# Optimization experiments

Hardware: AMD Instinct MI355X
Metric: run time of the kernel (lower is better)

Reference implementation:

```python
import jax, jax.numpy as jnp
import numpy as np

N, E = 50000, 1600000
IN, HID, HEADS, OUT = 128, 32, 4, 32
NEG_SLOPE = 0.2  # PyG GATConv default leaky_relu slope


def _glorot(k, shape):
    fan = shape[0] + shape[-1]
    return jax.random.normal(k, shape, dtype=jnp.float32) * np.sqrt(2.0 / fan).astype(np.float32)


def setup_inputs() -> dict:
    key = jax.random.key(0)
    ks = jax.random.split(key, 16)
    x = jax.random.normal(ks[0], (N, IN), dtype=jnp.float32)
    edge_index = jax.random.randint(ks[1], (2, E), 0, N, dtype=jnp.int32)
    # layer 0: in -> heads*hid, concat
    W0 = _glorot(ks[2], (IN, HEADS * HID))
    as0 = _glorot(ks[3], (HEADS, HID)); ad0 = _glorot(ks[4], (HEADS, HID))
    b0 = jnp.zeros((HEADS * HID,), jnp.float32)
    # layer 1: heads*hid -> heads*hid, concat
    W1 = _glorot(ks[5], (HEADS * HID, HEADS * HID))
    as1 = _glorot(ks[6], (HEADS, HID)); ad1 = _glorot(ks[7], (HEADS, HID))
    b1 = jnp.zeros((HEADS * HID,), jnp.float32)
    # layer 2: heads*hid -> out, heads=1, concat=False
    W2 = _glorot(ks[8], (HEADS * HID, OUT))
    as2 = _glorot(ks[9], (1, OUT)); ad2 = _glorot(ks[10], (1, OUT))
    b2 = jnp.zeros((OUT,), jnp.float32)
    return dict(x=x, edge_index=edge_index, W0=W0, as0=as0, ad0=ad0, b0=b0,
                W1=W1, as1=as1, ad1=ad1, b1=b1, W2=W2, as2=as2, ad2=ad2, b2=b2)


def gat_layer(x, src, dst, W, a_src, a_dst, b, heads, out_ch, concat):
    # linear transform per head: [N, heads, out_ch]
    h = (x @ W).reshape(N, heads, out_ch)
    # per-node attention half-logits: [N, heads]
    alpha_src = jnp.einsum('nhc,hc->nh', h, a_src)
    alpha_dst = jnp.einsum('nhc,hc->nh', h, a_dst)
    # per-edge logits (edge j -> i): [E', heads]
    logits = jax.nn.leaky_relu(alpha_src[src] + alpha_dst[dst], NEG_SLOPE)
    # segment softmax over incoming edges of each destination node
    m = jax.ops.segment_max(logits, dst, num_segments=N)
    e = jnp.exp(logits - m[dst])
    denom = jax.ops.segment_sum(e, dst, num_segments=N)
    alpha = e / denom[dst]
    # weighted message scatter-add: [N, heads, out_ch]
    out = jax.ops.segment_sum(h[src] * alpha[:, :, None], dst, num_segments=N)
    out = out.reshape(N, heads * out_ch) if concat else out.mean(axis=1)
    return out + b, alpha


def reference(x, edge_index, W0, as0, ad0, b0, W1, as1, ad1, b1, W2, as2, ad2, b2):
    # add self loops (PyG add_self_loops=True)
    loops = jnp.arange(N, dtype=edge_index.dtype)
    src = jnp.concatenate([edge_index[0], loops])
    dst = jnp.concatenate([edge_index[1], loops])

    h, alpha0 = gat_layer(x, src, dst, W0, as0, ad0, b0, HEADS, HID, True)
    h = jax.nn.elu(h)  # dropout inactive in eval mode
    h, _ = gat_layer(h, src, dst, W1, as1, ad1, b1, HEADS, HID, True)
    h = jax.nn.elu(h)
    out, _ = gat_layer(h, src, dst, W2, as2, ad2, b2, 1, OUT, False)
    return alpha0, out
```

## Files before the change

### kernel.cpp

```cpp
#include <hip/hip_runtime.h>
#include <math.h>

#define NN 50000
#define NEG 0.2f
#define TILE 4096

typedef __attribute__((ext_vector_type(8))) short short8;
typedef __attribute__((ext_vector_type(4))) float f32x4;

__device__ __forceinline__ unsigned short f2bf(float f){
    unsigned u = __float_as_uint(f);
    u += 0x7fffu + ((u >> 16) & 1u);
    return (unsigned short)(u >> 16);
}
__device__ __forceinline__ float bf2f(unsigned short v){
    return __uint_as_float(((unsigned)v) << 16);
}

__device__ __forceinline__ int excl_scan_256(int v, int* buf, int tid){
    buf[tid] = v;
    __syncthreads();
#pragma unroll
    for (int off = 1; off < 256; off <<= 1){
        int t = (tid >= off) ? buf[tid - off] : 0;
        __syncthreads();
        buf[tid] += t;
        __syncthreads();
    }
    return buf[tid] - v;
}

__global__ __launch_bounds__(256) void k_binning(const int* __restrict__ ei, int E,
        int* __restrict__ bucketCount, unsigned* __restrict__ tmp){
    __shared__ unsigned stage[TILE];
    __shared__ int hist[256], sbuf[256], exs[256], cur[256], gbase[256];
    int tid = threadIdx.x;
    int EP = E + NN;
    int tileBase = blockIdx.x * TILE;
    int cnt = min(TILE, EP - tileBase);

    hist[tid] = 0;
    __syncthreads();

    unsigned packed[16];
#pragma unroll
    for (int k = 0; k < 16; ++k){
        int e = tileBase + tid + (k << 8);
        unsigned p = 0xffffffffu;
        if (e < EP){
            int s, d;
            if (e < E){ s = ei[e]; d = ei[E + e]; } else { s = e - E; d = s; }
            p = ((unsigned)d << 16) | (unsigned)s;
            atomicAdd(&hist[d >> 8], 1);
        }
        packed[k] = p;
    }
    __syncthreads();
    int h = hist[tid];
    int ex = excl_scan_256(h, sbuf, tid);
    exs[tid] = ex;
    cur[tid] = ex;
    __syncthreads();
#pragma unroll
    for (int k = 0; k < 16; ++k){
        unsigned p = packed[k];
        if (p != 0xffffffffu){
            int b = p >> 24;
            int pos = atomicAdd(&cur[b], 1);
            stage[pos] = p;
        }
    }
    gbase[tid] = atomicAdd(&bucketCount[tid], h);
    __syncthreads();
    for (int i = tid; i < cnt; i += 256){
        unsigned p = stage[i];
        int b = p >> 24;
        tmp[(b << 14) + gbase[b] + (i - exs[b])] = p;
    }
}

__global__ __launch_bounds__(256) void k_bucket_csr(int EP,
        const int* __restrict__ bucketCount, const unsigned* __restrict__ tmp,
        int* __restrict__ row_ptr, unsigned short* __restrict__ ssrc){
    __shared__ int sbuf[256], deg[256], cur[256];
    __shared__ int baseSh, nSh;
    int b = blockIdx.x;
    int tid = threadIdx.x;
    int c = bucketCount[tid];
    int exb = excl_scan_256(c, sbuf, tid);
    if (tid == b){ baseSh = exb; nSh = c; }
    deg[tid] = 0;
    __syncthreads();
    int base = baseSh, n = nSh;
    const unsigned* tb = tmp + ((size_t)b << 14);
    for (int i = tid; i < n; i += 256)
        atomicAdd(&deg[(tb[i] >> 16) & 255], 1);
    __syncthreads();
    int d = deg[tid];
    int dx = excl_scan_256(d, sbuf, tid);
    cur[tid] = dx;
    int dst = (b << 8) + tid;
    if (dst < NN) row_ptr[dst] = base + dx;
    if (b == 0 && tid == 0) row_ptr[NN] = EP;
    __syncthreads();
    for (int i = tid; i < n; i += 256){
        unsigned p = tb[i];
        int pos = atomicAdd(&cur[(p >> 16) & 255], 1);
        ssrc[base + pos] = (unsigned short)(p & 0xffffu);
    }
}

__global__ void k_packW(const float* __restrict__ W0, const float* __restrict__ W1,
                        const float* __restrict__ W2,
                        unsigned short* __restrict__ h0, unsigned short* __restrict__ l0,
                        unsigned short* __restrict__ h1, unsigned short* __restrict__ l1,
                        unsigned short* __restrict__ h2, unsigned short* __restrict__ l2){
    int t = blockIdx.x * 256 + threadIdx.x;
    const float* W; unsigned short *ph, *pl; int Ncol; int u;
    if (t < 16384){ W = W0; ph = h0; pl = l0; Ncol = 128; u = t; }
    else if (t < 32768){ W = W1; ph = h1; pl = l1; Ncol = 128; u = t - 16384; }
    else if (t < 36864){ W = W2; ph = h2; pl = l2; Ncol = 32;  u = t - 32768; }
    else return;
    int n = u >> 7, k = u & 127;
    float f = W[k * Ncol + n];
    unsigned short hi = f2bf(f);
    unsigned short lo = f2bf(f - bf2f(hi));
    ph[n * 128 + k] = hi;
    pl[n * 128 + k] = lo;
}

template<int NT, int HH>
__global__ __launch_bounds__(256) void k_gemm_mfma(
        const float* __restrict__ A,
        const unsigned short* __restrict__ Bhi,
        const unsigned short* __restrict__ Blo,
        float* __restrict__ C, unsigned short* __restrict__ Cbf,
        const float* __restrict__ a_s,
        const float* __restrict__ a_d,
        float* __restrict__ asrc, float* __restrict__ adst,
        float* __restrict__ asrc_i, float* __restrict__ adst_i, int M){
    const int Ncol = NT * 16;
    int wave = threadIdx.x >> 6;
    int lane = threadIdx.x & 63;
    int r    = lane & 15;
    int oct  = lane >> 4;
    int rowBase = blockIdx.x * 64 + wave * 16;

    f32x4 acc[NT];
#pragma unroll
    for (int c = 0; c < NT; ++c) acc[c] = (f32x4){0.f, 0.f, 0.f, 0.f};

    int lrow = rowBase + r; if (lrow > M - 1) lrow = M - 1;
    const float* arow = A + (size_t)lrow * 128;

    for (int t = 0; t < 4; ++t){
        int k0 = t * 32 + oct * 8;
        float4 a0 = *(const float4*)&arow[k0];
        float4 a1 = *(const float4*)&arow[k0 + 4];
        float av[8] = {a0.x, a0.y, a0.z, a0.w, a1.x, a1.y, a1.z, a1.w};
        short8 ahi, alo;
#pragma unroll
        for (int j = 0; j < 8; ++j){
            unsigned short h = f2bf(av[j]);
            unsigned short l = f2bf(av[j] - bf2f(h));
            ahi[j] = (short)h; alo[j] = (short)l;
        }
#pragma unroll
        for (int c = 0; c < NT; ++c){
            short8 bhi = *(const short8*)&Bhi[(c * 16 + r) * 128 + k0];
            short8 blo = *(const short8*)&Blo[(c * 16 + r) * 128 + k0];
            acc[c] = __builtin_amdgcn_mfma_f32_16x16x32_bf16(ahi, bhi, acc[c], 0, 0, 0);
            acc[c] = __builtin_amdgcn_mfma_f32_16x16x32_bf16(alo, bhi, acc[c], 0, 0, 0);
            acc[c] = __builtin_amdgcn_mfma_f32_16x16x32_bf16(ahi, blo, acc[c], 0, 0, 0);
        }
    }
#pragma unroll
    for (int c = 0; c < NT; ++c){
#pragma unroll
        for (int reg = 0; reg < 4; ++reg){
            int row = rowBase + oct * 4 + reg;
            if (row < M){
                int colg = c * 16 + r;
                float v = acc[c][reg];
                if (C)   C[(size_t)row * Ncol + colg] = v;
                if (Cbf) Cbf[(size_t)(colg >> 5) * ((size_t)M * 32)
                             + (size_t)row * 32 + (colg & 31)] = f2bf(v);
            }
        }
    }

    float as_v[NT], ad_v[NT];
#pragma unroll
    for (int c = 0; c < NT; ++c){
        as_v[c] = a_s[c * 16 + r];
        ad_v[c] = a_d[c * 16 + r];
    }
    float vs[HH * 4], vd[HH * 4];
#pragma unroll
    for (int h = 0; h < HH; ++h)
#pragma unroll
        for (int reg = 0; reg < 4; ++reg){
            vs[h * 4 + reg] = acc[2 * h][reg] * as_v[2 * h]
                            + acc[2 * h + 1][reg] * as_v[2 * h + 1];
            vd[h * 4 + reg] = acc[2 * h][reg] * ad_v[2 * h]
                            + acc[2 * h + 1][reg] * ad_v[2 * h + 1];
        }
#pragma unroll
    for (int off = 1; off < 16; off <<= 1){
#pragma unroll
        for (int k = 0; k < HH * 4; ++k){
            vs[k] += __shfl_xor(vs[k], off);
            vd[k] += __shfl_xor(vd[k], off);
        }
    }
    if (HH == 4){
        int reg = r & 3, hd = r >> 2;
        int row = rowBase + oct * 4 + reg;
        if (row < M){
            asrc[hd * M + row] = vs[hd * 4 + reg];
            adst[hd * M + row] = vd[hd * 4 + reg];
            if (asrc_i){
                asrc_i[row * 4 + hd] = vs[hd * 4 + reg];
                adst_i[row * 4 + hd] = vd[hd * 4 + reg];
            }
        }
    } else {
        int reg = r & 3;
        int row = rowBase + oct * 4 + reg;
        if (row < M){
            if (r < 4)       asrc[row] = vs[reg];
            else if (r < 8)  adst[row] = vd[reg];
        }
    }
}

__global__ __launch_bounds__(256) void k_aggh4(
        const uint4* __restrict__ hb4,
        const float* __restrict__ asrc,
        const float* __restrict__ adst,
        const int* __restrict__ row_ptr, const unsigned short* __restrict__ ssrc,
        const float* __restrict__ bias, float* __restrict__ outp,
        float* __restrict__ gdenom, int writeStats){
    int b  = blockIdx.x;
    int h  = (b >> 1) & 3;
    int kh = (b >> 3) * 2 + (b & 1);
    int wave = threadIdx.x >> 6;
    int lane = threadIdx.x & 63;
    int ns = lane >> 4;
    int g  = (lane >> 2) & 3;
    int q  = lane & 3;
    int i  = kh * 16 + wave * 4 + ns;
    bool valid = (i < NN);
    int iv = valid ? i : NN - 1;
    int lo = row_ptr[iv], hi = row_ptr[iv + 1];
    float adv = adst[h * NN + iv];
    const uint4* hp = hb4 + (size_t)h * ((size_t)NN * 4);
    const float* ap = asrc + h * NN;

    float acc[8];
#pragma unroll
    for (int k = 0; k < 8; ++k) acc[k] = 0.f;
    float dsum = 0.f;

#define AGH_FMA(AA, GV) {                                                     \
        acc[0] += (AA) * __uint_as_float((GV).x << 16);                       \
        acc[1] += (AA) * __uint_as_float((GV).x & 0xffff0000u);               \
        acc[2] += (AA) * __uint_as_float((GV).y << 16);                       \
        acc[3] += (AA) * __uint_as_float((GV).y & 0xffff0000u);               \
        acc[4] += (AA) * __uint_as_float((GV).z << 16);                       \
        acc[5] += (AA) * __uint_as_float((GV).z & 0xffff0000u);               \
        acc[6] += (AA) * __uint_as_float((GV).w << 16);                       \
        acc[7] += (AA) * __uint_as_float((GV).w & 0xffff0000u); }
#define AGH_ONE(JJ) {                                                         \
        float lg_ = ap[(JJ)] + adv;                                           \
        lg_ = fmaxf(lg_, NEG * lg_);                                          \
        float a_ = __expf(lg_);                                               \
        dsum += a_;                                                           \
        uint4 gv_ = hp[(JJ) * 4u + (unsigned)q];                              \
        AGH_FMA(a_, gv_) }

    int idx = lo;
    if (lo & 1){
        if (g == 0){ unsigned j = ssrc[lo]; AGH_ONE(j) }
        idx = lo + 1;
    }
    for (; idx + 16 <= hi; idx += 16){
        unsigned pA = *(const unsigned*)&ssrc[idx + 2 * g];
        unsigned pB = *(const unsigned*)&ssrc[idx + 8 + 2 * g];
        unsigned j0 = pA & 0xffffu, j1 = pA >> 16;
        unsigned j2 = pB & 0xffffu, j3 = pB >> 16;
        float s0 = ap[j0], s1 = ap[j1], s2 = ap[j2], s3 = ap[j3];
        uint4 v0 = hp[j0 * 4u + (unsigned)q];
        uint4 v1 = hp[j1 * 4u + (unsigned)q];
        uint4 v2 = hp[j2 * 4u + (unsigned)q];
        uint4 v3 = hp[j3 * 4u + (unsigned)q];
        float lg0 = s0 + adv; lg0 = fmaxf(lg0, NEG * lg0);
        float lg1 = s1 + adv; lg1 = fmaxf(lg1, NEG * lg1);
        float lg2 = s2 + adv; lg2 = fmaxf(lg2, NEG * lg2);
        float lg3 = s3 + adv; lg3 = fmaxf(lg3, NEG * lg3);
        float a0 = __expf(lg0), a1 = __expf(lg1);
        float a2 = __expf(lg2), a3 = __expf(lg3);
        dsum += (a0 + a1) + (a2 + a3);
        AGH_FMA(a0, v0)
        AGH_FMA(a1, v1)
        AGH_FMA(a2, v2)
        AGH_FMA(a3, v3)
    }
    if (idx + 8 <= hi){
        unsigned pA = *(const unsigned*)&ssrc[idx + 2 * g];
        unsigned j0 = pA & 0xffffu, j1 = pA >> 16;
        float s0 = ap[j0], s1 = ap[j1];
        uint4 v0 = hp[j0 * 4u + (unsigned)q];
        uint4 v1 = hp[j1 * 4u + (unsigned)q];
        float lg0 = s0 + adv; lg0 = fmaxf(lg0, NEG * lg0);
        float lg1 = s1 + adv; lg1 = fmaxf(lg1, NEG * lg1);
        float a0 = __expf(lg0), a1 = __expf(lg1);
        dsum += a0 + a1;
        AGH_FMA(a0, v0)
        AGH_FMA(a1, v1)
        idx += 8;
    }
    {
        int k0 = idx + 2 * g, k1 = k0 + 1;
        if (k0 < hi){ unsigned j = ssrc[k0]; AGH_ONE(j) }
        if (k1 < hi){ unsigned j = ssrc[k1]; AGH_ONE(j) }
    }
#undef AGH_ONE
#undef AGH_FMA
#pragma unroll
    for (int k = 0; k < 8; ++k){
        acc[k] += __shfl_xor(acc[k], 4);
        acc[k] += __shfl_xor(acc[k], 8);
    }
    dsum += __shfl_xor(dsum, 4);
    dsum += __shfl_xor(dsum, 8);

    if (writeStats && g == 0 && q == 0 && valid)
        gdenom[i * 4 + h] = dsum;

    if (g == 0 && valid){
        float rs = 1.f / dsum;
        int c0 = h * 32 + q * 8;
        float4 bA = *(const float4*)&bias[c0];
        float4 bB = *(const float4*)&bias[c0 + 4];
        float o[8] = {acc[0] * rs + bA.x, acc[1] * rs + bA.y,
                      acc[2] * rs + bA.z, acc[3] * rs + bA.w,
                      acc[4] * rs + bB.x, acc[5] * rs + bB.y,
                      acc[6] * rs + bB.z, acc[7] * rs + bB.w};
#pragma unroll
        for (int k = 0; k < 8; ++k)
            o[k] = (o[k] > 0.f) ? o[k] : (__expf(o[k]) - 1.f);
        *(float4*)&outp[(size_t)i * 128 + c0]     = make_float4(o[0], o[1], o[2], o[3]);
        *(float4*)&outp[(size_t)i * 128 + c0 + 4] = make_float4(o[4], o[5], o[6], o[7]);
    }
}

__global__ void k_alpha0(const int* __restrict__ ei, int E,
                         const float4* __restrict__ asrc4, const float4* __restrict__ adst4,
                         const float4* __restrict__ gd4, float4* __restrict__ out){
    int e = blockIdx.x * 256 + threadIdx.x;
    int EP = E + NN;
    if (e >= EP) return;
    int s, d;
    if (e < E){ s = ei[e]; d = ei[E + e]; } else { s = e - E; d = s; }
    float4 as = asrc4[s], ad = adst4[d], dn = gd4[d];
    float4 r;
    float lg;
    lg = as.x + ad.x; lg = fmaxf(lg, NEG * lg); r.x = __expf(lg) / dn.x;
    lg = as.y + ad.y; lg = fmaxf(lg, NEG * lg); r.y = __expf(lg) / dn.y;
    lg = as.z + ad.z; lg = fmaxf(lg, NEG * lg); r.z = __expf(lg) / dn.z;
    lg = as.w + ad.w; lg = fmaxf(lg, NEG * lg); r.w = __expf(lg) / dn.w;
    out[e] = r;
}

__global__ __launch_bounds__(256) void k_agg1s(
        const float4* __restrict__ h24,
        const float* __restrict__ asrc, const float* __restrict__ adst,
        const int* __restrict__ row_ptr, const unsigned short* __restrict__ ssrc,
        const float* __restrict__ bias, float* __restrict__ outp){
    int wave = (blockIdx.x * 256 + threadIdx.x) >> 6;
    int lane = threadIdx.x & 63;
    if (wave >= NN) return;
    int i = wave;
    int lo = row_ptr[i], hi = row_ptr[i + 1];
    int g = lane >> 3;
    int q = lane & 7;
    float adv = adst[i];

    float acc[4] = {0.f, 0.f, 0.f, 0.f};
    float dsum = 0.f;

#define AGG1_ONE(JJ) {                                                        \
        float lg_ = asrc[(JJ)] + adv;                                         \
        lg_ = fmaxf(lg_, NEG * lg_);                                          \
        float a_ = __expf(lg_);                                               \
        dsum += a_;                                                           \
        float4 v_ = h24[(JJ) * 8u + (unsigned)q];                             \
        acc[0] += a_ * v_.x; acc[1] += a_ * v_.y;                             \
        acc[2] += a_ * v_.z; acc[3] += a_ * v_.w; }

    int idx = lo;
    if (lo & 1){
        if (g == 0){ unsigned j = ssrc[lo]; AGG1_ONE(j) }
        idx = lo + 1;
    }
    for (; idx + 16 <= hi; idx += 16){
        unsigned pair = *(const unsigned*)&ssrc[idx + 2 * g];
        unsigned j0 = pair & 0xffffu, j1 = pair >> 16;
        float s0 = asrc[j0];
        float s1 = asrc[j1];
        float4 v0 = h24[j0 * 8u + (unsigned)q];
        float4 v1 = h24[j1 * 8u + (unsigned)q];
        float lg0 = s0 + adv; lg0 = fmaxf(lg0, NEG * lg0);
        float lg1 = s1 + adv; lg1 = fmaxf(lg1, NEG * lg1);
        float a0 = __expf(lg0), a1 = __expf(lg1);
        dsum += a0 + a1;
        acc[0] += a0 * v0.x; acc[1] += a0 * v0.y;
        acc[2] += a0 * v0.z; acc[3] += a0 * v0.w;
        acc[0] += a1 * v1.x; acc[1] += a1 * v1.y;
        acc[2] += a1 * v1.z; acc[3] += a1 * v1.w;
    }
    {
        int k0 = idx + 2 * g, k1 = k0 + 1;
        if (k0 < hi){ unsigned j = ssrc[k0]; AGG1_ONE(j) }
        if (k1 < hi){ unsigned j = ssrc[k1]; AGG1_ONE(j) }
    }
#undef AGG1_ONE
#pragma unroll
    for (int k = 0; k < 4; ++k){
        acc[k] += __shfl_xor(acc[k], 8);
        acc[k] += __shfl_xor(acc[k], 16);
        acc[k] += __shfl_xor(acc[k], 32);
    }
    dsum += __shfl_xor(dsum, 8);
    dsum += __shfl_xor(dsum, 16);
    dsum += __shfl_xor(dsum, 32);
    if (g == 0){
        float rs = 1.f / dsum;
        float4 b = *(const float4*)&bias[q * 4];
        *(float4*)&outp[(size_t)i * 32 + q * 4] =
            make_float4(acc[0] * rs + b.x, acc[1] * rs + b.y,
                        acc[2] * rs + b.z, acc[3] * rs + b.w);
    }
}

extern "C" void kernel_launch(void* const* d_in, const int* in_sizes, int n_in,
                              void* d_out, int out_size, void* d_ws, size_t ws_size,
                              hipStream_t stream){
    const float* x   = (const float*)d_in[0];
    const int*   ei  = (const int*)  d_in[1];
    const float* W0  = (const float*)d_in[2];
    const float* as0 = (const float*)d_in[3];
    const float* ad0 = (const float*)d_in[4];
    const float* b0  = (const float*)d_in[5];
    const float* W1  = (const float*)d_in[6];
    const float* as1 = (const float*)d_in[7];
    const float* ad1 = (const float*)d_in[8];
    const float* b1  = (const float*)d_in[9];
    const float* W2  = (const float*)d_in[10];
    const float* as2 = (const float*)d_in[11];
    const float* ad2 = (const float*)d_in[12];
    const float* b2  = (const float*)d_in[13];

    const int E  = in_sizes[1] / 2;
    const int EP = E + NN;

    char* w = (char*)d_ws;
    size_t off = 0;
    auto carve = [&](size_t bytes) -> char* {
        char* p = w + off;
        off += (bytes + 255) & ~(size_t)255;
        return p;
    };
    int*            bucketCount = (int*)       carve(sizeof(int) * 256);
    int*            row_ptr = (int*)           carve(sizeof(int) * (NN + 1));
    unsigned short* ssrc    = (unsigned short*)carve(sizeof(short) * ((size_t)EP + 2));
    float*          hbuf    = (float*)         carve(sizeof(float) * (size_t)NN * 32);
    unsigned short* hb16    = (unsigned short*)carve(sizeof(short) * (size_t)NN * 128);
    float*          post    = (float*)         carve(sizeof(float) * (size_t)NN * 128);
    float*          asrc    = (float*)         carve(sizeof(float) * NN * 4);
    float*          adst    = (float*)         carve(sizeof(float) * NN * 4);
    float*          asrci   = (float*)         carve(sizeof(float) * NN * 4);
    float*          adsti   = (float*)         carve(sizeof(float) * NN * 4);
    float*          gdenom  = (float*)         carve(sizeof(float) * NN * 4);
    unsigned short* Whi0    = (unsigned short*)carve(sizeof(short) * 16384);
    unsigned short* Wlo0    = (unsigned short*)carve(sizeof(short) * 16384);
    unsigned short* Whi1    = (unsigned short*)carve(sizeof(short) * 16384);
    unsigned short* Wlo1    = (unsigned short*)carve(sizeof(short) * 16384);
    unsigned short* Whi2    = (unsigned short*)carve(sizeof(short) * 4096);
    unsigned short* Wlo2    = (unsigned short*)carve(sizeof(short) * 4096);
    unsigned*       tmp     = (unsigned*)post;

    float* out_alpha = (float*)d_out;
    float* out_final = (float*)d_out + (size_t)EP * 4;

    const int edgeBlocks = (EP + 255) / 256;
    const int waveBlocks = (NN + 3) / 4;
    const int aggBlocks  = 12504;
    const int gemmBlocks = (NN + 63) / 64;

    hipMemsetAsync(bucketCount, 0, sizeof(int) * 256, stream);
    k_binning   <<<(EP + TILE - 1) / TILE, 256, 0, stream>>>(ei, E, bucketCount, tmp);
    k_bucket_csr<<<256, 256, 0, stream>>>(EP, bucketCount, tmp, row_ptr, ssrc);
    k_packW     <<<144, 256, 0, stream>>>(W0, W1, W2, Whi0, Wlo0, Whi1, Wlo1, Whi2, Wlo2);

    k_gemm_mfma<8, 4><<<gemmBlocks, 256, 0, stream>>>(x, Whi0, Wlo0,
        nullptr, hb16, as0, ad0, asrc, adst, asrci, adsti, NN);
    k_aggh4<<<aggBlocks, 256, 0, stream>>>((const uint4*)hb16, asrc, adst, row_ptr,
                                           ssrc, b0, post, gdenom, 1);
    k_alpha0<<<edgeBlocks, 256, 0, stream>>>(ei, E, (const float4*)asrci,
                                             (const float4*)adsti,
                                             (const float4*)gdenom, (float4*)out_alpha);

    k_gemm_mfma<8, 4><<<gemmBlocks, 256, 0, stream>>>(post, Whi1, Wlo1,
        nullptr, hb16, as1, ad1, asrc, adst, nullptr, nullptr, NN);
    k_aggh4<<<aggBlocks, 256, 0, stream>>>((const uint4*)hb16, asrc, adst, row_ptr,
                                           ssrc, b1, post, gdenom, 0);

    k_gemm_mfma<2, 1><<<gemmBlocks, 256, 0, stream>>>(post, Whi2, Wlo2,
        hbuf, nullptr, as2, ad2, asrc, adst, nullptr, nullptr, NN);
    k_agg1s<<<waveBlocks, 256, 0, stream>>>((const float4*)hbuf, asrc, adst, row_ptr,
                                            ssrc, b2, out_final);
}
```

Measured before the change: 423.9 us.

## Remap aggregation lanes: 8 nodes per wave in heads, planar split for final layer

```diff
diff --git a/kernel.cpp b/kernel.cpp
--- a/kernel.cpp
+++ b/kernel.cpp
@@ -182,7 +182,13 @@
             if (row < M){
                 int colg = c * 16 + r;
                 float v = acc[c][reg];
-                if (C)   C[(size_t)row * Ncol + colg] = v;
+                if (C){
+                    if (NT == 2)
+                        C[(size_t)(colg >> 4) * ((size_t)M * 16)
+                          + (size_t)row * 16 + (colg & 15)] = v;
+                    else
+                        C[(size_t)row * Ncol + colg] = v;
+                }
                 if (Cbf) Cbf[(size_t)(colg >> 5) * ((size_t)M * 32)
                              + (size_t)row * 32 + (colg & 31)] = f2bf(v);
             }
@@ -234,7 +240,7 @@
     }
 }
 
-__global__ __launch_bounds__(256) void k_aggh4(
+__global__ __launch_bounds__(256) void k_aggh8(
         const uint4* __restrict__ hb4,
         const float* __restrict__ asrc,
         const float* __restrict__ adst,
@@ -246,10 +252,10 @@
     int kh = (b >> 3) * 2 + (b & 1);
     int wave = threadIdx.x >> 6;
     int lane = threadIdx.x & 63;
-    int ns = lane >> 4;
-    int g  = (lane >> 2) & 3;
+    int ns = lane >> 3;
+    int g  = (lane >> 2) & 1;
     int q  = lane & 3;
-    int i  = kh * 16 + wave * 4 + ns;
+    int i  = kh * 32 + wave * 8 + ns;
     bool valid = (i < NN);
     int iv = valid ? i : NN - 1;
     int lo = row_ptr[iv], hi = row_ptr[iv + 1];
@@ -284,9 +290,9 @@
         if (g == 0){ unsigned j = ssrc[lo]; AGH_ONE(j) }
         idx = lo + 1;
     }
-    for (; idx + 16 <= hi; idx += 16){
+    for (; idx + 8 <= hi; idx += 8){
         unsigned pA = *(const unsigned*)&ssrc[idx + 2 * g];
-        unsigned pB = *(const unsigned*)&ssrc[idx + 8 + 2 * g];
+        unsigned pB = *(const unsigned*)&ssrc[idx + 4 + 2 * g];
         unsigned j0 = pA & 0xffffu, j1 = pA >> 16;
         unsigned j2 = pB & 0xffffu, j3 = pB >> 16;
         float s0 = ap[j0], s1 = ap[j1], s2 = ap[j2], s3 = ap[j3];
@@ -306,7 +312,7 @@
         AGH_FMA(a2, v2)
         AGH_FMA(a3, v3)
     }
-    if (idx + 8 <= hi){
+    if (idx + 4 <= hi){
         unsigned pA = *(const unsigned*)&ssrc[idx + 2 * g];
         unsigned j0 = pA & 0xffffu, j1 = pA >> 16;
         float s0 = ap[j0], s1 = ap[j1];
@@ -318,7 +324,7 @@
         dsum += a0 + a1;
         AGH_FMA(a0, v0)
         AGH_FMA(a1, v1)
-        idx += 8;
+        idx += 4;
     }
     {
         int k0 = idx + 2 * g, k1 = k0 + 1;
@@ -328,12 +334,9 @@
 #undef AGH_ONE
 #undef AGH_FMA
 #pragma unroll
-    for (int k = 0; k < 8; ++k){
+    for (int k = 0; k < 8; ++k)
         acc[k] += __shfl_xor(acc[k], 4);
-        acc[k] += __shfl_xor(acc[k], 8);
-    }
     dsum += __shfl_xor(dsum, 4);
-    dsum += __shfl_xor(dsum, 8);
 
     if (writeStats && g == 0 && q == 0 && valid)
         gdenom[i * 4 + h] = dsum;
@@ -373,74 +376,103 @@
     out[e] = r;
 }
 
-__global__ __launch_bounds__(256) void k_agg1s(
-        const float4* __restrict__ h24,
+__global__ __launch_bounds__(256) void k_agg1p(
+        const float4* __restrict__ hpl,
         const float* __restrict__ asrc, const float* __restrict__ adst,
         const int* __restrict__ row_ptr, const unsigned short* __restrict__ ssrc,
         const float* __restrict__ bias, float* __restrict__ outp){
-    int wave = (blockIdx.x * 256 + threadIdx.x) >> 6;
+    int b  = blockIdx.x;
+    int p  = (b >> 2) & 1;
+    int kp = (b >> 3) * 4 + (b & 3);
+    int wave = threadIdx.x >> 6;
     int lane = threadIdx.x & 63;
-    if (wave >= NN) return;
-    int i = wave;
-    int lo = row_ptr[i], hi = row_ptr[i + 1];
-    int g = lane >> 3;
-    int q = lane & 7;
-    float adv = adst[i];
+    int ns = lane >> 4;
+    int g  = (lane >> 2) & 3;
+    int q  = lane & 3;
+    int i  = kp * 16 + wave * 4 + ns;
+    bool valid = (i < NN);
+    int iv = valid ? i : NN - 1;
+    int lo = row_ptr[iv], hi = row_ptr[iv + 1];
+    float adv = adst[iv];
+    const float4* hp = hpl + (size_t)p * ((size_t)NN * 4);
 
     float acc[4] = {0.f, 0.f, 0.f, 0.f};
     float dsum = 0.f;
 
-#define AGG1_ONE(JJ) {                                                        \
+#define AG1_FMA(AA, VV) {                                                     \
+        acc[0] += (AA) * (VV).x; acc[1] += (AA) * (VV).y;                     \
+        acc[2] += (AA) * (VV).z; acc[3] += (AA) * (VV).w; }
+#define AG1_ONE(JJ) {                                                         \
         float lg_ = asrc[(JJ)] + adv;                                         \
         lg_ = fmaxf(lg_, NEG * lg_);                                          \
         float a_ = __expf(lg_);                                               \
         dsum += a_;                                                           \
-        float4 v_ = h24[(JJ) * 8u + (unsigned)q];                             \
-        acc[0] += a_ * v_.x; acc[1] += a_ * v_.y;                             \
-        acc[2] += a_ * v_.z; acc[3] += a_ * v_.w; }
+        float4 v_ = hp[(JJ) * 4u + (unsigned)q];                              \
+        AG1_FMA(a_, v_) }
 
     int idx = lo;
     if (lo & 1){
-        if (g == 0){ unsigned j = ssrc[lo]; AGG1_ONE(j) }
+        if (g == 0){ unsigned j = ssrc[lo]; AG1_ONE(j) }
         idx = lo + 1;
     }
     for (; idx + 16 <= hi; idx += 16){
-        unsigned pair = *(const unsigned*)&ssrc[idx + 2 * g];
-        unsigned j0 = pair & 0xffffu, j1 = pair >> 16;
-        float s0 = asrc[j0];
-        float s1 = asrc[j1];
-        float4 v0 = h24[j0 * 8u + (unsigned)q];
-        float4 v1 = h24[j1 * 8u + (unsigned)q];
+        unsigned pA = *(const unsigned*)&ssrc[idx + 2 * g];
+        unsigned pB = *(const unsigned*)&ssrc[idx + 8 + 2 * g];
+        unsigned j0 = pA & 0xffffu, j1 = pA >> 16;
+        unsigned j2 = pB & 0xffffu, j3 = pB >> 16;
+        float s0 = asrc[j0], s1 = asrc[j1], s2 = asrc[j2], s3 = asrc[j3];
+        float4 v0 = hp[j0 * 4u + (unsigned)q];
+        float4 v1 = hp[j1 * 4u + (unsigned)q];
+        float4 v2 = hp[j2 * 4u + (unsigned)q];
+        float4 v3 = hp[j3 * 4u + (unsigned)q];
+        float lg0 = s0 + adv; lg0 = fmaxf(lg0, NEG * lg0);
+        float lg1 = s1 + adv; lg1 = fmaxf(lg1, NEG * lg1);
+        float lg2 = s2 + adv; lg2 = fmaxf(lg2, NEG * lg2);
+        float lg3 = s3 + adv; lg3 = fmaxf(lg3, NEG * lg3);
+        float a0 = __expf(lg0), a1 = __expf(lg1);
+        float a2 = __expf(lg2), a3 = __expf(lg3);
+        dsum += (a0 + a1) + (a2 + a3);
+        AG1_FMA(a0, v0)
+        AG1_FMA(a1, v1)
+        AG1_FMA(a2, v2)
+        AG1_FMA(a3, v3)
+    }
+    if (idx + 8 <= hi){
+        unsigned pA = *(const unsigned*)&ssrc[idx + 2 * g];
+        unsigned j0 = pA & 0xffffu, j1 = pA >> 16;
+        float s0 = asrc[j0], s1 = asrc[j1];
+        float4 v0 = hp[j0 * 4u + (unsigned)q];
+        float4 v1 = hp[j1 * 4u + (unsigned)q];
         float lg0 = s0 + adv; lg0 = fmaxf(lg0, NEG * lg0);
         float lg1 = s1 + adv; lg1 = fmaxf(lg1, NEG * lg1);
         float a0 = __expf(lg0), a1 = __expf(lg1);
         dsum += a0 + a1;
-        acc[0] += a0 * v0.x; acc[1] += a0 * v0.y;
-        acc[2] += a0 * v0.z; acc[3] += a0 * v0.w;
-        acc[0] += a1 * v1.x; acc[1] += a1 * v1.y;
-        acc[2] += a1 * v1.z; acc[3] += a1 * v1.w;
+        AG1_FMA(a0, v0)
+        AG1_FMA(a1, v1)
+        idx += 8;
     }
     {
         int k0 = idx + 2 * g, k1 = k0 + 1;
-        if (k0 < hi){ unsigned j = ssrc[k0]; AGG1_ONE(j) }
-        if (k1 < hi){ unsigned j = ssrc[k1]; AGG1_ONE(j) }
-    }
-#undef AGG1_ONE
+        if (k0 < hi){ unsigned j = ssrc[k0]; AG1_ONE(j) }
+        if (k1 < hi){ unsigned j = ssrc[k1]; AG1_ONE(j) }
+    }
+#undef AG1_ONE
+#undef AG1_FMA
 #pragma unroll
     for (int k = 0; k < 4; ++k){
+        acc[k] += __shfl_xor(acc[k], 4);
         acc[k] += __shfl_xor(acc[k], 8);
-        acc[k] += __shfl_xor(acc[k], 16);
-        acc[k] += __shfl_xor(acc[k], 32);
-    }
+    }
+    dsum += __shfl_xor(dsum, 4);
     dsum += __shfl_xor(dsum, 8);
-    dsum += __shfl_xor(dsum, 16);
-    dsum += __shfl_xor(dsum, 32);
-    if (g == 0){
+
+    if (g == 0 && valid){
         float rs = 1.f / dsum;
-        float4 b = *(const float4*)&bias[q * 4];
-        *(float4*)&outp[(size_t)i * 32 + q * 4] =
-            make_float4(acc[0] * rs + b.x, acc[1] * rs + b.y,
-                        acc[2] * rs + b.z, acc[3] * rs + b.w);
+        int c0 = p * 16 + q * 4;
+        float4 bv = *(const float4*)&bias[c0];
+        *(float4*)&outp[(size_t)i * 32 + c0] =
+            make_float4(acc[0] * rs + bv.x, acc[1] * rs + bv.y,
+                        acc[2] * rs + bv.z, acc[3] * rs + bv.w);
     }
 }
 
@@ -495,8 +527,8 @@
     float* out_final = (float*)d_out + (size_t)EP * 4;
 
     const int edgeBlocks = (EP + 255) / 256;
-    const int waveBlocks = (NN + 3) / 4;
-    const int aggBlocks  = 12504;
+    const int aggBlocks  = 6256;
+    const int agg1Blocks = 6256;
     const int gemmBlocks = (NN + 63) / 64;
 
     hipMemsetAsync(bucketCount, 0, sizeof(int) * 256, stream);
@@ -506,7 +538,7 @@
 
     k_gemm_mfma<8, 4><<<gemmBlocks, 256, 0, stream>>>(x, Whi0, Wlo0,
         nullptr, hb16, as0, ad0, asrc, adst, asrci, adsti, NN);
-    k_aggh4<<<aggBlocks, 256, 0, stream>>>((const uint4*)hb16, asrc, adst, row_ptr,
+    k_aggh8<<<aggBlocks, 256, 0, stream>>>((const uint4*)hb16, asrc, adst, row_ptr,
                                            ssrc, b0, post, gdenom, 1);
     k_alpha0<<<edgeBlocks, 256, 0, stream>>>(ei, E, (const float4*)asrci,
                                              (const float4*)adsti,
@@ -514,11 +546,11 @@
 
     k_gemm_mfma<8, 4><<<gemmBlocks, 256, 0, stream>>>(post, Whi1, Wlo1,
         nullptr, hb16, as1, ad1, asrc, adst, nullptr, nullptr, NN);
-    k_aggh4<<<aggBlocks, 256, 0, stream>>>((const uint4*)hb16, asrc, adst, row_ptr,
+    k_aggh8<<<aggBlocks, 256, 0, stream>>>((const uint4*)hb16, asrc, adst, row_ptr,
                                            ssrc, b1, post, gdenom, 0);
 
     k_gemm_mfma<2, 1><<<gemmBlocks, 256, 0, stream>>>(post, Whi2, Wlo2,
         hbuf, nullptr, as2, ad2, asrc, adst, nullptr, nullptr, NN);
-    k_agg1s<<<waveBlocks, 256, 0, stream>>>((const float4*)hbuf, asrc, adst, row_ptr,
+    k_agg1p<<<agg1Blocks, 256, 0, stream>>>((const float4*)hbuf, asrc, adst, row_ptr,
                                             ssrc, b2, out_final);
 }
```

Result: no change. 431.5 us (+1.8%).

## Store layer-2 features in bf16 and aggregate four nodes per wave

Applied to the files above, without the earlier changes.

```diff
diff --git a/kernel.cpp b/kernel.cpp
--- a/kernel.cpp
+++ b/kernel.cpp
@@ -373,74 +373,111 @@
     out[e] = r;
 }
 
-__global__ __launch_bounds__(256) void k_agg1s(
-        const float4* __restrict__ h24,
+__global__ __launch_bounds__(256) void k_agg1b(
+        const uint4* __restrict__ hb,
         const float* __restrict__ asrc, const float* __restrict__ adst,
         const int* __restrict__ row_ptr, const unsigned short* __restrict__ ssrc,
         const float* __restrict__ bias, float* __restrict__ outp){
-    int wave = (blockIdx.x * 256 + threadIdx.x) >> 6;
+    int wave = threadIdx.x >> 6;
     int lane = threadIdx.x & 63;
-    if (wave >= NN) return;
-    int i = wave;
-    int lo = row_ptr[i], hi = row_ptr[i + 1];
-    int g = lane >> 3;
-    int q = lane & 7;
-    float adv = adst[i];
-
-    float acc[4] = {0.f, 0.f, 0.f, 0.f};
+    int ns = lane >> 4;
+    int g  = (lane >> 2) & 3;
+    int q  = lane & 3;
+    int i  = blockIdx.x * 16 + wave * 4 + ns;
+    bool valid = (i < NN);
+    int iv = valid ? i : NN - 1;
+    int lo = row_ptr[iv], hi = row_ptr[iv + 1];
+    float adv = adst[iv];
+
+    float acc[8];
+#pragma unroll
+    for (int k = 0; k < 8; ++k) acc[k] = 0.f;
     float dsum = 0.f;
 
-#define AGG1_ONE(JJ) {                                                        \
+#define AGB_FMA(AA, GV) {                                                     \
+        acc[0] += (AA) * __uint_as_float((GV).x << 16);                       \
+        acc[1] += (AA) * __uint_as_float((GV).x & 0xffff0000u);               \
+        acc[2] += (AA) * __uint_as_float((GV).y << 16);                       \
+        acc[3] += (AA) * __uint_as_float((GV).y & 0xffff0000u);               \
+        acc[4] += (AA) * __uint_as_float((GV).z << 16);                       \
+        acc[5] += (AA) * __uint_as_float((GV).z & 0xffff0000u);               \
+        acc[6] += (AA) * __uint_as_float((GV).w << 16);                       \
+        acc[7] += (AA) * __uint_as_float((GV).w & 0xffff0000u); }
+#define AGB_ONE(JJ) {                                                         \
         float lg_ = asrc[(JJ)] + adv;                                         \
         lg_ = fmaxf(lg_, NEG * lg_);                                          \
         float a_ = __expf(lg_);                                               \
         dsum += a_;                                                           \
-        float4 v_ = h24[(JJ) * 8u + (unsigned)q];                             \
-        acc[0] += a_ * v_.x; acc[1] += a_ * v_.y;                             \
-        acc[2] += a_ * v_.z; acc[3] += a_ * v_.w; }
+        uint4 gv_ = hb[(JJ) * 4u + (unsigned)q];                              \
+        AGB_FMA(a_, gv_) }
 
     int idx = lo;
     if (lo & 1){
-        if (g == 0){ unsigned j = ssrc[lo]; AGG1_ONE(j) }
+        if (g == 0){ unsigned j = ssrc[lo]; AGB_ONE(j) }
         idx = lo + 1;
     }
     for (; idx + 16 <= hi; idx += 16){
-        unsigned pair = *(const unsigned*)&ssrc[idx + 2 * g];
-        unsigned j0 = pair & 0xffffu, j1 = pair >> 16;
-        float s0 = asrc[j0];
-        float s1 = asrc[j1];
-        float4 v0 = h24[j0 * 8u + (unsigned)q];
-        float4 v1 = h24[j1 * 8u + (unsigned)q];
+        unsigned pA = *(const unsigned*)&ssrc[idx + 2 * g];
+        unsigned pB = *(const unsigned*)&ssrc[idx + 8 + 2 * g];
+        unsigned j0 = pA & 0xffffu, j1 = pA >> 16;
+        unsigned j2 = pB & 0xffffu, j3 = pB >> 16;
+        float s0 = asrc[j0], s1 = asrc[j1], s2 = asrc[j2], s3 = asrc[j3];
+        uint4 v0 = hb[j0 * 4u + (unsigned)q];
+        uint4 v1 = hb[j1 * 4u + (unsigned)q];
+        uint4 v2 = hb[j2 * 4u + (unsigned)q];
+        uint4 v3 = hb[j3 * 4u + (unsigned)q];
+        float lg0 = s0 + adv; lg0 = fmaxf(lg0, NEG * lg0);
+        float lg1 = s1 + adv; lg1 = fmaxf(lg1, NEG * lg1);
+        float lg2 = s2 + adv; lg2 = fmaxf(lg2, NEG * lg2);
+        float lg3 = s3 + adv; lg3 = fmaxf(lg3, NEG * lg3);
+        float a0 = __expf(lg0), a1 = __expf(lg1);
+        float a2 = __expf(lg2), a3 = __expf(lg3);
+        dsum += (a0 + a1) + (a2 + a3);
+        AGB_FMA(a0, v0)
+        AGB_FMA(a1, v1)
+        AGB_FMA(a2, v2)
+        AGB_FMA(a3, v3)
+    }
+    if (idx + 8 <= hi){
+        unsigned pA = *(const unsigned*)&ssrc[idx + 2 * g];
+        unsigned j0 = pA & 0xffffu, j1 = pA >> 16;
+        float s0 = asrc[j0], s1 = asrc[j1];
+        uint4 v0 = hb[j0 * 4u + (unsigned)q];
+        uint4 v1 = hb[j1 * 4u + (unsigned)q];
         float lg0 = s0 + adv; lg0 = fmaxf(lg0, NEG * lg0);
         float lg1 = s1 + adv; lg1 = fmaxf(lg1, NEG * lg1);
         float a0 = __expf(lg0), a1 = __expf(lg1);
         dsum += a0 + a1;
-        acc[0] += a0 * v0.x; acc[1] += a0 * v0.y;
-        acc[2] += a0 * v0.z; acc[3] += a0 * v0.w;
-        acc[0] += a1 * v1.x; acc[1] += a1 * v1.y;
-        acc[2] += a1 * v1.z; acc[3] += a1 * v1.w;
+        AGB_FMA(a0, v0)
+        AGB_FMA(a1, v1)
+        idx += 8;
     }
     {
         int k0 = idx + 2 * g, k1 = k0 + 1;
-        if (k0 < hi){ unsigned j = ssrc[k0]; AGG1_ONE(j) }
-        if (k1 < hi){ unsigned j = ssrc[k1]; AGG1_ONE(j) }
-    }
-#undef AGG1_ONE
-#pragma unroll
-    for (int k = 0; k < 4; ++k){
+        if (k0 < hi){ unsigned j = ssrc[k0]; AGB_ONE(j) }
+        if (k1 < hi){ unsigned j = ssrc[k1]; AGB_ONE(j) }
+    }
+#undef AGB_ONE
+#undef AGB_FMA
+#pragma unroll
+    for (int k = 0; k < 8; ++k){
+        acc[k] += __shfl_xor(acc[k], 4);
         acc[k] += __shfl_xor(acc[k], 8);
-        acc[k] += __shfl_xor(acc[k], 16);
-        acc[k] += __shfl_xor(acc[k], 32);
-    }
+    }
+    dsum += __shfl_xor(dsum, 4);
     dsum += __shfl_xor(dsum, 8);
-    dsum += __shfl_xor(dsum, 16);
-    dsum += __shfl_xor(dsum, 32);
-    if (g == 0){
+
+    if (g == 0 && valid){
         float rs = 1.f / dsum;
-        float4 b = *(const float4*)&bias[q * 4];
-        *(float4*)&outp[(size_t)i * 32 + q * 4] =
-            make_float4(acc[0] * rs + b.x, acc[1] * rs + b.y,
-                        acc[2] * rs + b.z, acc[3] * rs + b.w);
+        int c0 = q * 8;
+        float4 bA = *(const float4*)&bias[c0];
+        float4 bB = *(const float4*)&bias[c0 + 4];
+        *(float4*)&outp[(size_t)i * 32 + c0] =
+            make_float4(acc[0] * rs + bA.x, acc[1] * rs + bA.y,
+                        acc[2] * rs + bA.z, acc[3] * rs + bA.w);
+        *(float4*)&outp[(size_t)i * 32 + c0 + 4] =
+            make_float4(acc[4] * rs + bB.x, acc[5] * rs + bB.y,
+                        acc[6] * rs + bB.z, acc[7] * rs + bB.w);
     }
 }
 
@@ -475,7 +512,7 @@
     int*            bucketCount = (int*)       carve(sizeof(int) * 256);
     int*            row_ptr = (int*)           carve(sizeof(int) * (NN + 1));
     unsigned short* ssrc    = (unsigned short*)carve(sizeof(short) * ((size_t)EP + 2));
-    float*          hbuf    = (float*)         carve(sizeof(float) * (size_t)NN * 32);
+    unsigned short* hb2     = (unsigned short*)carve(sizeof(short) * (size_t)NN * 32);
     unsigned short* hb16    = (unsigned short*)carve(sizeof(short) * (size_t)NN * 128);
     float*          post    = (float*)         carve(sizeof(float) * (size_t)NN * 128);
     float*          asrc    = (float*)         carve(sizeof(float) * NN * 4);
@@ -495,8 +532,8 @@
     float* out_final = (float*)d_out + (size_t)EP * 4;
 
     const int edgeBlocks = (EP + 255) / 256;
-    const int waveBlocks = (NN + 3) / 4;
     const int aggBlocks  = 12504;
+    const int agg1Blocks = (NN + 15) / 16;
     const int gemmBlocks = (NN + 63) / 64;
 
     hipMemsetAsync(bucketCount, 0, sizeof(int) * 256, stream);
@@ -518,7 +555,7 @@
                                            ssrc, b1, post, gdenom, 0);
 
     k_gemm_mfma<2, 1><<<gemmBlocks, 256, 0, stream>>>(post, Whi2, Wlo2,
-        hbuf, nullptr, as2, ad2, asrc, adst, nullptr, nullptr, NN);
-    k_agg1s<<<waveBlocks, 256, 0, stream>>>((const float4*)hbuf, asrc, adst, row_ptr,
+        nullptr, hb2, as2, ad2, asrc, adst, nullptr, nullptr, NN);
+    k_agg1b<<<agg1Blocks, 256, 0, stream>>>((const uint4*)hb2, asrc, adst, row_ptr,
                                             ssrc, b2, out_final);
 }
```

Measured after the change: 411.6 us. -2.9%, faster.
